# Kernel optimization log

Hardware: AMD Instinct MI355X
Metric: run time of the kernel (lower is better)

Reference implementation:

```python
import jax, jax.numpy as jnp
import numpy as np

N_NODES = 100000
N_EDGES = 3200000
N_FEATS = 512
HIDDEN = 16
N_CLASSES = 40


def gcn_conv(x, edge_index, W, b):
    """PyG-style GCNConv: linear -> symmetric-normalized scatter-add -> bias."""
    n = x.shape[0]
    src, dst = edge_index[0], edge_index[1]
    # add self-loops
    loop = jnp.arange(n, dtype=src.dtype)
    src = jnp.concatenate([src, loop])
    dst = jnp.concatenate([dst, loop])
    # symmetric normalization deg^{-1/2}[src] * deg^{-1/2}[dst]
    deg = jax.ops.segment_sum(jnp.ones_like(src, dtype=x.dtype), dst, num_segments=n)
    dinv = jnp.where(deg > 0, jax.lax.rsqrt(jnp.maximum(deg, 1.0)), 0.0)
    norm = dinv[src] * dinv[dst]  # [E+N]
    h = x @ W                     # [N, out]
    msg = h[src] * norm[:, None]  # gather + scale, [E+N, out]
    out = jax.ops.segment_sum(msg, dst, num_segments=n)  # scatter-add at targets
    return out + b


def setup_inputs() -> dict:
    key = jax.random.key(0)
    k1, k2, k3, k4 = jax.random.split(key, 4)
    x = jax.random.normal(k1, (N_NODES, N_FEATS), dtype=jnp.float32)
    edge_index = jax.random.randint(k2, (2, N_EDGES), 0, N_NODES, dtype=jnp.int64)
    # Glorot-ish scaled weights
    W1 = jax.random.normal(k3, (N_FEATS, HIDDEN), dtype=jnp.float32) * (1.0 / np.sqrt(N_FEATS))
    b1 = jnp.zeros((HIDDEN,), dtype=jnp.float32)
    W2 = jax.random.normal(k4, (HIDDEN, N_CLASSES), dtype=jnp.float32) * (1.0 / np.sqrt(HIDDEN))
    b2 = jnp.zeros((N_CLASSES,), dtype=jnp.float32)
    return {"x": x, "edge_index": edge_index, "W1": W1, "b1": b1, "W2": W2, "b2": b2}


def reference(x, edge_index, W1, b1, W2, b2):
    h = gcn_conv(x, edge_index, W1, b1)
    h = jax.nn.relu(h)
    # dropout is identity in eval mode
    h = gcn_conv(h, edge_index, W2, b2)
    return jax.nn.log_softmax(h, axis=1)
```

## Files before the change

kernel.cpp:

```cpp
#include <hip/hip_runtime.h>
#include <hip/hip_bf16.h>

#define NN 100000
#define NE 3200000
#define NF 512
#define NH 16
#define NC 40
#define NB 782
#define CAP 5120
#define NBLK 128
#define CHUNK 25000
#define GEMMB 1563

typedef __attribute__((ext_vector_type(4))) float f32x4;
typedef __attribute__((ext_vector_type(8))) short bf16x8;

static __device__ __forceinline__ unsigned short f2b(float f) {
    unsigned int u = __float_as_uint(f);
    u += 0x7FFFu + ((u >> 16) & 1u);
    return (unsigned short)(u >> 16);
}
static __device__ __forceinline__ float b2f(unsigned short u) {
    return __uint_as_float(((unsigned int)u) << 16);
}


__global__ void __launch_bounds__(256) kA_gemm_hist(const float* __restrict__ x,
                                                    const float* __restrict__ W1,
                                                    const int* __restrict__ ei,
                                                    unsigned short* __restrict__ h1,
                                                    int* __restrict__ histG) {
    __shared__ int smem[4096];
    if (blockIdx.x < GEMMB) {
        unsigned short* wl = (unsigned short*)smem;
        for (int idx = threadIdx.x; idx < 8192; idx += 256) {
            int s = idx >> 9;
            int l = (idx >> 3) & 63;
            int e = idx & 7;
            int k = s * 32 + (l >> 4) * 8 + e;
            wl[idx] = f2b(W1[k * 16 + (l & 15)]);
        }
        __syncthreads();
        int wave = threadIdx.x >> 6;
        int l = threadIdx.x & 63;
        int m0 = blockIdx.x * 64 + wave * 16;
        if (m0 >= NN) return;
        int row = m0 + (l & 15);
        int krow = (l >> 4) * 8;
        const float* xr = x + (size_t)row * NF + krow;
        const unsigned short* wf = wl + l * 8;
        f32x4 acc = {0.f, 0.f, 0.f, 0.f};
#pragma unroll 4
        for (int s = 0; s < 16; ++s) {
            f32x4 xa = *(const f32x4*)(xr + s * 32);
            f32x4 xb = *(const f32x4*)(xr + s * 32 + 4);
            union { bf16x8 v; unsigned short u[8]; } a;
            a.u[0] = f2b(xa.x); a.u[1] = f2b(xa.y); a.u[2] = f2b(xa.z); a.u[3] = f2b(xa.w);
            a.u[4] = f2b(xb.x); a.u[5] = f2b(xb.y); a.u[6] = f2b(xb.z); a.u[7] = f2b(xb.w);
            bf16x8 b = *(const bf16x8*)(wf + s * 512);
            acc = __builtin_amdgcn_mfma_f32_16x16x32_bf16(a.v, b, acc, 0, 0, 0);
        }
#pragma unroll
        for (int r = 0; r < 4; ++r) {
            int orow = m0 + (l >> 4) * 4 + r;
            h1[(size_t)orow * NH + (l & 15)] = f2b(acc[r]);
        }
    } else {
        int* h = smem;
        for (int i = threadIdx.x; i < NB; i += 256) h[i] = 0;
        __syncthreads();
        int b = blockIdx.x - GEMMB;
        int e0 = b * CHUNK, e1 = min(NE, e0 + CHUNK);
        for (int e = e0 + threadIdx.x; e < e1; e += 256)
            atomicAdd(&h[((unsigned)ei[NE + e]) >> 7], 1);
        __syncthreads();
        for (int i = threadIdx.x; i < NB; i += 256)
            histG[b * NB + i] = h[i];
    }
}


__global__ void __launch_bounds__(256) k_colscan(const int* __restrict__ histG,
                                                 int* __restrict__ ofsG,
                                                 int* __restrict__ bcnt) {
    __shared__ int sh[256];
    int t = threadIdx.x;
    int k = blockIdx.x * 2 + (t >> 7);
    int tt = t & 127;
    int v = histG[tt * NB + k];
    sh[t] = v;
    __syncthreads();
    for (int off = 1; off < 128; off <<= 1) {
        int add = (tt >= off) ? sh[t - off] : 0;
        __syncthreads();
        sh[t] += add;
        __syncthreads();
    }
    ofsG[k * NBLK + tt] = sh[t] - v;
    if (tt == 127) bcnt[k] = sh[t];
}


__global__ void k_bscan(const int* __restrict__ bcnt, int* __restrict__ bptr,
                        int* __restrict__ rowptr) {
    __shared__ int sh[1024];
    int t = threadIdx.x;
    int v = (t < NB) ? bcnt[t] : 0;
    sh[t] = v;
    __syncthreads();
    for (int off = 1; off < 1024; off <<= 1) {
        int add = (t >= off) ? sh[t - off] : 0;
        __syncthreads();
        sh[t] += add;
        __syncthreads();
    }
    if (t < NB) bptr[t] = sh[t] - v;
    if (t == 0) { bptr[NB] = NE; rowptr[NN] = NE; }
}


__global__ void __launch_bounds__(1024) k_msscatter(const int* __restrict__ ei,
                                                    const int* __restrict__ bptr,
                                                    const int* __restrict__ ofsG,
                                                    unsigned int* __restrict__ pairs) {
    __shared__ int lcur[NB];
    int b = blockIdx.x;
    for (int k = threadIdx.x; k < NB; k += 1024)
        lcur[k] = bptr[k] + ofsG[k * NBLK + b];
    __syncthreads();
    int e0 = b * CHUNK, e1 = min(NE, e0 + CHUNK);
    for (int e = e0 + threadIdx.x; e < e1; e += 1024) {
        unsigned int s = (unsigned int)ei[e];
        unsigned int d = (unsigned int)ei[NE + e];
        int pos = atomicAdd(&lcur[d >> 7], 1);
        pairs[pos] = s | ((d & 127u) << 17);
    }
}


__global__ void __launch_bounds__(256) k_bsort(const unsigned int* __restrict__ pairs,
                                               const int* __restrict__ bptr,
                                               int* __restrict__ rowptr,
                                               float* __restrict__ dinv,
                                               int* __restrict__ ssrc) {
    __shared__ unsigned int ein[CAP];
    __shared__ unsigned int srt[CAP];
    __shared__ int lcnt[128], lofs[128], lcur[128];
    int b = blockIdx.x;
    int s0 = bptr[b], s1 = bptr[b + 1];
    int n = s1 - s0;
    for (int i = threadIdx.x; i < n; i += 256) ein[i] = pairs[s0 + i];
    if (threadIdx.x < 128) lcnt[threadIdx.x] = 0;
    __syncthreads();
    for (int i = threadIdx.x; i < n; i += 256) atomicAdd(&lcnt[ein[i] >> 17], 1);
    __syncthreads();
    if (threadIdx.x < 128) lofs[threadIdx.x] = lcnt[threadIdx.x];
    __syncthreads();
    for (int off = 1; off < 128; off <<= 1) {
        int add = 0;
        if (threadIdx.x < 128 && threadIdx.x >= off) add = lofs[threadIdx.x - off];
        __syncthreads();
        if (threadIdx.x < 128) lofs[threadIdx.x] += add;
        __syncthreads();
    }
    if (threadIdx.x < 128) {
        int excl = lofs[threadIdx.x] - lcnt[threadIdx.x];
        lcur[threadIdx.x] = excl;
        int node = b * 128 + threadIdx.x;
        if (node < NN) {
            rowptr[node] = s0 + excl;
            dinv[node] = rsqrtf((float)(lcnt[threadIdx.x] + 1));
        }
    }
    __syncthreads();
    for (int i = threadIdx.x; i < n; i += 256) {
        unsigned int v = ein[i];
        int pos = atomicAdd(&lcur[v >> 17], 1);
        srt[pos] = v & 0x1FFFFu;
    }
    __syncthreads();
    for (int i = threadIdx.x; i < n; i += 256) ssrc[s0 + i] = (int)srt[i];
}


__global__ void __launch_bounds__(256) k_agg1(const unsigned short* __restrict__ hs,
                                              const int* __restrict__ rowptr,
                                              const int* __restrict__ ssrc,
                                              const float* __restrict__ dinv,
                                              const float* __restrict__ b1,
                                              unsigned short* __restrict__ r1) {
    int l = threadIdx.x & 63;
    int node = blockIdx.x * 4 + (threadIdx.x >> 6);
    int j = l & 15;
    int ec = l >> 4;
    float di = dinv[node];
    int s = rowptr[node];
    int e1 = rowptr[node + 1];
    float acc = (ec == 0) ? b2f(hs[(size_t)node * NH + j]) * di : 0.0f;
#pragma unroll 4
    for (int e = s + ec; e < e1; e += 4) {
        int src = ssrc[e];
        acc += b2f(hs[(size_t)src * NH + j]) * dinv[src];
    }
    acc += __shfl_xor(acc, 16, 64);
    acc += __shfl_xor(acc, 32, 64);
    if (ec == 0) {
        float o = fmaxf(acc * di + b1[j], 0.0f) * di;
        r1[(size_t)node * NH + j] = f2b(o);
    }
}


__global__ void __launch_bounds__(256) k_agg2(const unsigned short* __restrict__ rs,
                                              const int* __restrict__ rowptr,
                                              const int* __restrict__ ssrc,
                                              const float* __restrict__ dinv,
                                              const float* __restrict__ W2,
                                              const float* __restrict__ b2,
                                              float* __restrict__ out) {
    __shared__ float w[NH * NC];
    __shared__ float bb[NC];
    int t = threadIdx.x;
    for (int i = t; i < NH * NC; i += 256) w[i] = W2[i];
    if (t < NC) bb[t] = b2[t];
    __syncthreads();
    int l = t & 63;
    int node = blockIdx.x * 4 + (t >> 6);
    int j = l & 15;
    int ec = l >> 4;
    float di = dinv[node];
    int s = rowptr[node];
    int e1 = rowptr[node + 1];
    float acc = (ec == 0) ? b2f(rs[(size_t)node * NH + j]) : 0.0f;
#pragma unroll 4
    for (int e = s + ec; e < e1; e += 4) {
        int src = ssrc[e];
        acc += b2f(rs[(size_t)src * NH + j]);
    }
    acc += __shfl_xor(acc, 16, 64);
    acc += __shfl_xor(acc, 32, 64);
    float zv = acc * di;
    float lg = (l < NC) ? bb[l] : -1e30f;
#pragma unroll
    for (int k = 0; k < NH; ++k) {
        float zk = __shfl(zv, k, 64);
        if (l < NC) lg += zk * w[k * NC + l];
    }
    float mx = lg;
#pragma unroll
    for (int off = 1; off < 64; off <<= 1) mx = fmaxf(mx, __shfl_xor(mx, off, 64));
    float ex = (l < NC) ? __expf(lg - mx) : 0.0f;
    float sm = ex;
#pragma unroll
    for (int off = 1; off < 64; off <<= 1) sm += __shfl_xor(sm, off, 64);
    if (l < NC) out[(size_t)node * NC + l] = lg - mx - __logf(sm);
}


extern "C" void kernel_launch(void* const* d_in, const int* in_sizes, int n_in,
                              void* d_out, int out_size, void* d_ws, size_t ws_size,
                              hipStream_t stream) {
    const float* x  = (const float*)d_in[0];
    const int*   ei = (const int*)d_in[1];
    const float* W1 = (const float*)d_in[2];
    const float* b1 = (const float*)d_in[3];
    const float* W2 = (const float*)d_in[4];
    const float* b2 = (const float*)d_in[5];
    float* out = (float*)d_out;

    char* ws = (char*)d_ws;
    size_t off = 0;
    auto alloc = [&](size_t bytes) -> void* {
        void* p = ws + off;
        off += (bytes + 255) & ~(size_t)255;
        return p;
    };
    int* histG      = (int*)alloc((size_t)NBLK * NB * 4);
    int* ofsG       = (int*)alloc((size_t)NB * NBLK * 4);
    int* bcnt       = (int*)alloc((size_t)NB * 4);
    int* bptr       = (int*)alloc((size_t)(NB + 1) * 4);
    int* rowptr     = (int*)alloc((size_t)(NN + 1) * 4);
    float* dinv     = (float*)alloc((size_t)NN * 4);
    unsigned int* pairs = (unsigned int*)alloc((size_t)NE * 4);
    int* ssrc       = (int*)alloc((size_t)NE * 4);
    unsigned short* h1  = (unsigned short*)alloc((size_t)NN * NH * 2);
    unsigned short* r1  = (unsigned short*)alloc((size_t)NN * NH * 2);

    kA_gemm_hist<<<GEMMB + NBLK, 256, 0, stream>>>(x, W1, ei, h1, histG);
    k_colscan<<<NB / 2, 256, 0, stream>>>(histG, ofsG, bcnt);
    k_bscan<<<1, 1024, 0, stream>>>(bcnt, bptr, rowptr);
    k_msscatter<<<NBLK, 1024, 0, stream>>>(ei, bptr, ofsG, pairs);
    k_bsort<<<NB, 256, 0, stream>>>(pairs, bptr, rowptr, dinv, ssrc);
    k_agg1<<<NN / 4, 256, 0, stream>>>(h1, rowptr, ssrc, dinv, b1, r1);
    k_agg2<<<NN / 4, 256, 0, stream>>>(r1, rowptr, ssrc, dinv, W2, b2, out);
}
```

Measured before the change: 257.9 us.

## Use finer 64-node buckets and fold histogram work into GEMM blocks

Halves the destination bucket width so there are 1563 buckets of 64 nodes, and splits the edges into 512 chunks instead of 128. This spreads the counting-sort scatter and the per-bucket sort over more, smaller blocks. The histogram is now computed by the first 512 GEMM blocks before they do their GEMM tile, rather than by a separate tail of blocks. The scans are reshaped to match: one 512-thread block per bucket for the column scan, and two elements per thread for the bucket scan. The trade-off is a larger histogram and offset matrix, plus a serial histogram phase on the GEMM blocks that may delay the GEMM.

```diff
diff --git a/kernel.cpp b/kernel.cpp
--- a/kernel.cpp
+++ b/kernel.cpp
@@ -6,10 +6,11 @@
 #define NF 512
 #define NH 16
 #define NC 40
-#define NB 782
-#define CAP 5120
-#define NBLK 128
-#define CHUNK 25000
+#define BKT_SH 6
+#define NBKT 1563
+#define CAP2 2560
+#define NBLK 512
+#define CHUNK 6250
 #define GEMMB 1563
 
 typedef __attribute__((ext_vector_type(4))) float f32x4;
@@ -31,73 +32,73 @@
                                                     unsigned short* __restrict__ h1,
                                                     int* __restrict__ histG) {
     __shared__ int smem[4096];
-    if (blockIdx.x < GEMMB) {
-        unsigned short* wl = (unsigned short*)smem;
-        for (int idx = threadIdx.x; idx < 8192; idx += 256) {
-            int s = idx >> 9;
-            int l = (idx >> 3) & 63;
-            int e = idx & 7;
-            int k = s * 32 + (l >> 4) * 8 + e;
-            wl[idx] = f2b(W1[k * 16 + (l & 15)]);
-        }
-        __syncthreads();
-        int wave = threadIdx.x >> 6;
-        int l = threadIdx.x & 63;
-        int m0 = blockIdx.x * 64 + wave * 16;
-        if (m0 >= NN) return;
-        int row = m0 + (l & 15);
-        int krow = (l >> 4) * 8;
-        const float* xr = x + (size_t)row * NF + krow;
-        const unsigned short* wf = wl + l * 8;
-        f32x4 acc = {0.f, 0.f, 0.f, 0.f};
+    int tid = threadIdx.x;
+    if (blockIdx.x < NBLK) {
+        int* h = smem;
+        for (int i = tid; i < NBKT; i += 256) h[i] = 0;
+        __syncthreads();
+        int b = blockIdx.x;
+        int e0 = b * CHUNK, e1 = min(NE, e0 + CHUNK);
+        for (int e = e0 + tid; e < e1; e += 256)
+            atomicAdd(&h[((unsigned)ei[NE + e]) >> BKT_SH], 1);
+        __syncthreads();
+        for (int i = tid; i < NBKT; i += 256)
+            histG[b * NBKT + i] = h[i];
+        __syncthreads();
+    }
+    unsigned short* wl = (unsigned short*)smem;
+    for (int idx = tid; idx < 8192; idx += 256) {
+        int s = idx >> 9;
+        int l = (idx >> 3) & 63;
+        int e = idx & 7;
+        int k = s * 32 + (l >> 4) * 8 + e;
+        wl[idx] = f2b(W1[k * 16 + (l & 15)]);
+    }
+    __syncthreads();
+    int wave = tid >> 6;
+    int l = tid & 63;
+    int m0 = blockIdx.x * 64 + wave * 16;
+    if (m0 >= NN) return;
+    int row = m0 + (l & 15);
+    int krow = (l >> 4) * 8;
+    const float* xr = x + (size_t)row * NF + krow;
+    const unsigned short* wf = wl + l * 8;
+    f32x4 acc = {0.f, 0.f, 0.f, 0.f};
 #pragma unroll 4
-        for (int s = 0; s < 16; ++s) {
-            f32x4 xa = *(const f32x4*)(xr + s * 32);
-            f32x4 xb = *(const f32x4*)(xr + s * 32 + 4);
-            union { bf16x8 v; unsigned short u[8]; } a;
-            a.u[0] = f2b(xa.x); a.u[1] = f2b(xa.y); a.u[2] = f2b(xa.z); a.u[3] = f2b(xa.w);
-            a.u[4] = f2b(xb.x); a.u[5] = f2b(xb.y); a.u[6] = f2b(xb.z); a.u[7] = f2b(xb.w);
-            bf16x8 b = *(const bf16x8*)(wf + s * 512);
-            acc = __builtin_amdgcn_mfma_f32_16x16x32_bf16(a.v, b, acc, 0, 0, 0);
-        }
+    for (int s = 0; s < 16; ++s) {
+        f32x4 xa = *(const f32x4*)(xr + s * 32);
+        f32x4 xb = *(const f32x4*)(xr + s * 32 + 4);
+        union { bf16x8 v; unsigned short u[8]; } a;
+        a.u[0] = f2b(xa.x); a.u[1] = f2b(xa.y); a.u[2] = f2b(xa.z); a.u[3] = f2b(xa.w);
+        a.u[4] = f2b(xb.x); a.u[5] = f2b(xb.y); a.u[6] = f2b(xb.z); a.u[7] = f2b(xb.w);
+        bf16x8 b = *(const bf16x8*)(wf + s * 512);
+        acc = __builtin_amdgcn_mfma_f32_16x16x32_bf16(a.v, b, acc, 0, 0, 0);
+    }
 #pragma unroll
-        for (int r = 0; r < 4; ++r) {
-            int orow = m0 + (l >> 4) * 4 + r;
-            h1[(size_t)orow * NH + (l & 15)] = f2b(acc[r]);
-        }
-    } else {
-        int* h = smem;
-        for (int i = threadIdx.x; i < NB; i += 256) h[i] = 0;
-        __syncthreads();
-        int b = blockIdx.x - GEMMB;
-        int e0 = b * CHUNK, e1 = min(NE, e0 + CHUNK);
-        for (int e = e0 + threadIdx.x; e < e1; e += 256)
-            atomicAdd(&h[((unsigned)ei[NE + e]) >> 7], 1);
-        __syncthreads();
-        for (int i = threadIdx.x; i < NB; i += 256)
-            histG[b * NB + i] = h[i];
-    }
-}
-
-
-__global__ void __launch_bounds__(256) k_colscan(const int* __restrict__ histG,
+    for (int r = 0; r < 4; ++r) {
+        int orow = m0 + (l >> 4) * 4 + r;
+        h1[(size_t)orow * NH + (l & 15)] = f2b(acc[r]);
+    }
+}
+
+
+__global__ void __launch_bounds__(512) k_colscan(const int* __restrict__ histG,
                                                  int* __restrict__ ofsG,
                                                  int* __restrict__ bcnt) {
-    __shared__ int sh[256];
+    __shared__ int sh[NBLK];
+    int k = blockIdx.x;
     int t = threadIdx.x;
-    int k = blockIdx.x * 2 + (t >> 7);
-    int tt = t & 127;
-    int v = histG[tt * NB + k];
+    int v = histG[t * NBKT + k];
     sh[t] = v;
     __syncthreads();
-    for (int off = 1; off < 128; off <<= 1) {
-        int add = (tt >= off) ? sh[t - off] : 0;
+    for (int off = 1; off < NBLK; off <<= 1) {
+        int add = (t >= off) ? sh[t - off] : 0;
         __syncthreads();
         sh[t] += add;
         __syncthreads();
     }
-    ofsG[k * NBLK + tt] = sh[t] - v;
-    if (tt == 127) bcnt[k] = sh[t];
+    ofsG[k * NBLK + t] = sh[t] - v;
+    if (t == NBLK - 1) bcnt[k] = sh[t];
 }
 
 
@@ -105,8 +106,11 @@
                         int* __restrict__ rowptr) {
     __shared__ int sh[1024];
     int t = threadIdx.x;
-    int v = (t < NB) ? bcnt[t] : 0;
-    sh[t] = v;
+    int i0 = 2 * t, i1 = 2 * t + 1;
+    int a = (i0 < NBKT) ? bcnt[i0] : 0;
+    int b = (i1 < NBKT) ? bcnt[i1] : 0;
+    int pair = a + b;
+    sh[t] = pair;
     __syncthreads();
     for (int off = 1; off < 1024; off <<= 1) {
         int add = (t >= off) ? sh[t - off] : 0;
@@ -114,26 +118,28 @@
         sh[t] += add;
         __syncthreads();
     }
-    if (t < NB) bptr[t] = sh[t] - v;
-    if (t == 0) { bptr[NB] = NE; rowptr[NN] = NE; }
-}
-
-
-__global__ void __launch_bounds__(1024) k_msscatter(const int* __restrict__ ei,
-                                                    const int* __restrict__ bptr,
-                                                    const int* __restrict__ ofsG,
-                                                    unsigned int* __restrict__ pairs) {
-    __shared__ int lcur[NB];
+    int excl = sh[t] - pair;
+    if (i0 < NBKT) bptr[i0] = excl;
+    if (i1 < NBKT) bptr[i1] = excl + a;
+    if (t == 0) { bptr[NBKT] = NE; rowptr[NN] = NE; }
+}
+
+
+__global__ void __launch_bounds__(512) k_msscatter(const int* __restrict__ ei,
+                                                   const int* __restrict__ bptr,
+                                                   const int* __restrict__ ofsG,
+                                                   unsigned int* __restrict__ pairs) {
+    __shared__ int lcur[NBKT];
     int b = blockIdx.x;
-    for (int k = threadIdx.x; k < NB; k += 1024)
+    for (int k = threadIdx.x; k < NBKT; k += 512)
         lcur[k] = bptr[k] + ofsG[k * NBLK + b];
     __syncthreads();
     int e0 = b * CHUNK, e1 = min(NE, e0 + CHUNK);
-    for (int e = e0 + threadIdx.x; e < e1; e += 1024) {
+    for (int e = e0 + threadIdx.x; e < e1; e += 512) {
         unsigned int s = (unsigned int)ei[e];
         unsigned int d = (unsigned int)ei[NE + e];
-        int pos = atomicAdd(&lcur[d >> 7], 1);
-        pairs[pos] = s | ((d & 127u) << 17);
+        int pos = atomicAdd(&lcur[d >> BKT_SH], 1);
+        pairs[pos] = s | ((d & 63u) << 17);
     }
 }
 
@@ -143,30 +149,30 @@
                                                int* __restrict__ rowptr,
                                                float* __restrict__ dinv,
                                                int* __restrict__ ssrc) {
-    __shared__ unsigned int ein[CAP];
-    __shared__ unsigned int srt[CAP];
-    __shared__ int lcnt[128], lofs[128], lcur[128];
+    __shared__ unsigned int ein[CAP2];
+    __shared__ unsigned int srt[CAP2];
+    __shared__ int lcnt[64], lofs[64], lcur[64];
     int b = blockIdx.x;
     int s0 = bptr[b], s1 = bptr[b + 1];
     int n = s1 - s0;
     for (int i = threadIdx.x; i < n; i += 256) ein[i] = pairs[s0 + i];
-    if (threadIdx.x < 128) lcnt[threadIdx.x] = 0;
+    if (threadIdx.x < 64) lcnt[threadIdx.x] = 0;
     __syncthreads();
     for (int i = threadIdx.x; i < n; i += 256) atomicAdd(&lcnt[ein[i] >> 17], 1);
     __syncthreads();
-    if (threadIdx.x < 128) lofs[threadIdx.x] = lcnt[threadIdx.x];
-    __syncthreads();
-    for (int off = 1; off < 128; off <<= 1) {
+    if (threadIdx.x < 64) lofs[threadIdx.x] = lcnt[threadIdx.x];
+    __syncthreads();
+    for (int off = 1; off < 64; off <<= 1) {
         int add = 0;
-        if (threadIdx.x < 128 && threadIdx.x >= off) add = lofs[threadIdx.x - off];
-        __syncthreads();
-        if (threadIdx.x < 128) lofs[threadIdx.x] += add;
-        __syncthreads();
-    }
-    if (threadIdx.x < 128) {
+        if (threadIdx.x < 64 && threadIdx.x >= off) add = lofs[threadIdx.x - off];
+        __syncthreads();
+        if (threadIdx.x < 64) lofs[threadIdx.x] += add;
+        __syncthreads();
+    }
+    if (threadIdx.x < 64) {
         int excl = lofs[threadIdx.x] - lcnt[threadIdx.x];
         lcur[threadIdx.x] = excl;
-        int node = b * 128 + threadIdx.x;
+        int node = b * 64 + threadIdx.x;
         if (node < NN) {
             rowptr[node] = s0 + excl;
             dinv[node] = rsqrtf((float)(lcnt[threadIdx.x] + 1));
@@ -275,10 +281,10 @@
         off += (bytes + 255) & ~(size_t)255;
         return p;
     };
-    int* histG      = (int*)alloc((size_t)NBLK * NB * 4);
-    int* ofsG       = (int*)alloc((size_t)NB * NBLK * 4);
-    int* bcnt       = (int*)alloc((size_t)NB * 4);
-    int* bptr       = (int*)alloc((size_t)(NB + 1) * 4);
+    int* histG      = (int*)alloc((size_t)NBLK * NBKT * 4);
+    int* ofsG       = (int*)alloc((size_t)NBKT * NBLK * 4);
+    int* bcnt       = (int*)alloc((size_t)NBKT * 4);
+    int* bptr       = (int*)alloc((size_t)(NBKT + 1) * 4);
     int* rowptr     = (int*)alloc((size_t)(NN + 1) * 4);
     float* dinv     = (float*)alloc((size_t)NN * 4);
     unsigned int* pairs = (unsigned int*)alloc((size_t)NE * 4);
@@ -286,11 +292,11 @@
     unsigned short* h1  = (unsigned short*)alloc((size_t)NN * NH * 2);
     unsigned short* r1  = (unsigned short*)alloc((size_t)NN * NH * 2);
 
-    kA_gemm_hist<<<GEMMB + NBLK, 256, 0, stream>>>(x, W1, ei, h1, histG);
-    k_colscan<<<NB / 2, 256, 0, stream>>>(histG, ofsG, bcnt);
+    kA_gemm_hist<<<GEMMB, 256, 0, stream>>>(x, W1, ei, h1, histG);
+    k_colscan<<<NBKT, NBLK, 0, stream>>>(histG, ofsG, bcnt);
     k_bscan<<<1, 1024, 0, stream>>>(bcnt, bptr, rowptr);
-    k_msscatter<<<NBLK, 1024, 0, stream>>>(ei, bptr, ofsG, pairs);
-    k_bsort<<<NB, 256, 0, stream>>>(pairs, bptr, rowptr, dinv, ssrc);
+    k_msscatter<<<NBLK, 512, 0, stream>>>(ei, bptr, ofsG, pairs);
+    k_bsort<<<NBKT, 256, 0, stream>>>(pairs, bptr, rowptr, dinv, ssrc);
     k_agg1<<<NN / 4, 256, 0, stream>>>(h1, rowptr, ssrc, dinv, b1, r1);
     k_agg2<<<NN / 4, 256, 0, stream>>>(r1, rowptr, ssrc, dinv, W2, b2, out);
 }
```

Measured after the change: 255.3 us. Within noise of the previous version (-1.0%).
